# Optimization experiments

Hardware: AMD Instinct MI355X
Metric: run time of the kernel (lower is better)

## Reference

```python
import jax, jax.numpy as jnp
import numpy as np
from jax.scipy.linalg import expm

DIM = 2048        # state dimension (init arg `dim`)
M_STEPS = 8192    # kernel length (init arg `timestamp`)
DELTA = 0.01      # ZOH step size (init arg `delta`)
STAB = 1e-3       # stabilizer added to A before inversion (matches torch code)


def setup_inputs() -> dict:
    key = jax.random.key(0)
    k1, k2, k3 = jax.random.split(key, 3)
    # Match the torch init scaling so matrix_exp/inv stay well-conditioned.
    A = jnp.eye(DIM, dtype=jnp.float32) * -0.01 \
        + jax.random.normal(k1, (DIM, DIM), dtype=jnp.float32) * 0.001
    B = jax.random.normal(k2, (DIM, 1), dtype=jnp.float32) * 0.01
    C = jax.random.normal(k3, (1, DIM), dtype=jnp.float32) * 0.01
    return {"A": A, "B": B, "C": C, "M": M_STEPS}


def reference(A, B, C, M):
    dim = A.shape[0]
    I = jnp.eye(dim, dtype=A.dtype)
    # --- ZOH discretization (torch._zoh_discretize) ---
    A_bar = expm(DELTA * A)                         # [dim, dim]
    A_inv = jnp.linalg.inv(A + STAB * I)            # [dim, dim]
    B_bar = A_inv @ (A_bar - I) @ (DELTA * B)       # [dim, 1]

    # --- kernel power iteration (torch._compute_K_bar) ---
    # K[t] = C @ A_bar^t @ B_bar. Since B_bar is a vector, the serial
    # matrix-power loop reduces to M sequential matvecs (same math).
    def step(x, _):
        term = (C @ x)[0, 0]        # scalar K_t
        return A_bar @ x, term      # advance state: A_bar^{t+1} B_bar

    _, terms = jax.lax.scan(step, B_bar, None, length=M)  # [M]
    K_bar = terms[::-1][None, :]    # flip along time, shape [1, M]
    return K_bar
```

## Files before the change

### kernel.cpp

```cpp
#include <hip/hip_runtime.h>


#define DIMN 2048
#define MSTEPS 8192
#define RSPLIT 91
#define NSTEPS 90
#define NN ((size_t)DIMN * DIMN)
#define SCRD ((size_t)(1024*1024 + 512*512 + 256*256 + 128*128 + 64*64))
#define NBLK 32

__global__ __launch_bounds__(256)
void k_combine4(float* out,
                const float* i1, float c1, const float* i2, float c2,
                const float* i3, float c3, const float* i4, float c4,
                float dval)
{
  const int total = DIMN * DIMN;
  for (int idx = blockIdx.x * 256 + threadIdx.x; idx < total; idx += gridDim.x * 256) {
    float v = 0.f;
    if (i1) v = fmaf(c1, i1[idx], v);
    if (i2) v = fmaf(c2, i2[idx], v);
    if (i3) v = fmaf(c3, i3[idx], v);
    if (i4) v = fmaf(c4, i4[idx], v);
    if ((idx >> 11) == (idx & 2047)) v += dval;
    out[idx] = v;
  }
}

__global__ __launch_bounds__(256)
void k_fill64(const float* __restrict__ A, double* __restrict__ M)
{
  const int total = DIMN * DIMN;
  for (int idx = blockIdx.x * 256 + threadIdx.x; idx < total; idx += gridDim.x * 256) {
    double v = (double)A[idx];
    if ((idx >> 11) == (idx & 2047)) v += 1e-3;
    M[idx] = v;
  }
}

#define GBM 128
#define GBN 128
#define GBK 8
__global__ __launch_bounds__(256)
void k_gemm(const float* __restrict__ A, int lda,
            const float* __restrict__ B, int ldb,
            float* C, int ldc, int K, float alpha,
            const float* E1, int ld1, float c1,
            const float* E2, int ld2, float c2,
            const float* E3, int ld3, float c3,
            float dval)
{
  __shared__ float As[GBK][GBM];
  __shared__ float Bs[GBK][GBN];
  const int tid = threadIdx.x;
  const int tx = tid & 15, ty = tid >> 4;
  const int brow = blockIdx.y * GBM, bcol = blockIdx.x * GBN;

  const int arow = tid >> 1, ac0 = (tid & 1) * 4;
  const int brw  = tid >> 5, bc0 = (tid & 31) * 4;

  const float* Aptr = A + (size_t)(brow + arow) * lda + ac0;
  const float* Bptr = B + (size_t)brw * ldb + (bcol + bc0);

  float4 aPre = *(const float4*)Aptr;
  float4 bPre = *(const float4*)Bptr;

  float acc[8][8];
#pragma unroll
  for (int i = 0; i < 8; ++i)
#pragma unroll
    for (int j = 0; j < 8; ++j) acc[i][j] = 0.f;

  const int nk = K / GBK;
  for (int kt = 0; kt < nk; ++kt) {
    As[ac0 + 0][arow] = aPre.x;
    As[ac0 + 1][arow] = aPre.y;
    As[ac0 + 2][arow] = aPre.z;
    As[ac0 + 3][arow] = aPre.w;
    *(float4*)&Bs[brw][bc0] = bPre;
    __syncthreads();
    if (kt + 1 < nk) {
      aPre = *(const float4*)(Aptr + (size_t)(kt + 1) * GBK);
      bPre = *(const float4*)(Bptr + (size_t)(kt + 1) * GBK * ldb);
    }
#pragma unroll
    for (int kk = 0; kk < GBK; ++kk) {
      float a[8], b[8];
      *(float4*)&a[0] = *(const float4*)&As[kk][ty * 8];
      *(float4*)&a[4] = *(const float4*)&As[kk][ty * 8 + 4];
      *(float4*)&b[0] = *(const float4*)&Bs[kk][tx * 8];
      *(float4*)&b[4] = *(const float4*)&Bs[kk][tx * 8 + 4];
#pragma unroll
      for (int i = 0; i < 8; ++i)
#pragma unroll
        for (int j = 0; j < 8; ++j)
          acc[i][j] = fmaf(a[i], b[j], acc[i][j]);
    }
    __syncthreads();
  }
#pragma unroll
  for (int i = 0; i < 8; ++i) {
    const int gi = brow + ty * 8 + i;
#pragma unroll
    for (int j = 0; j < 8; ++j) {
      const int gj = bcol + tx * 8 + j;
      float v = alpha * acc[i][j];
      if (E1) v = fmaf(c1, E1[(size_t)gi * ld1 + gj], v);
      if (E2) v = fmaf(c2, E2[(size_t)gi * ld2 + gj], v);
      if (E3) v = fmaf(c3, E3[(size_t)gi * ld3 + gj], v);
      if (gi == gj) v += dval;
      C[(size_t)gi * ldc + gj] = v;
    }
  }
}

#define DBM 64
#define DBK 8
__global__ __launch_bounds__(256)
void k_dgemm(const double* __restrict__ A, int lda,
             const double* __restrict__ B, int ldb,
             double* C, int ldc, int K, double alpha,
             const double* E1, int ld1, double c1)
{
  __shared__ double As[DBK][DBM];
  __shared__ double Bs[DBK][DBM];
  const int tid = threadIdx.x;
  const int tx = tid & 15, ty = tid >> 4;
  const int brow = blockIdx.y * DBM, bcol = blockIdx.x * DBM;

  const int arow = tid >> 2, ac0 = (tid & 3) * 2;
  const int brw  = tid >> 5, bc0 = (tid & 31) * 2;

  const double* Aptr = A + (size_t)(brow + arow) * lda + ac0;
  const double* Bptr = B + (size_t)brw * ldb + (bcol + bc0);

  double2 aPre = *(const double2*)Aptr;
  double2 bPre = *(const double2*)Bptr;

  double acc[4][4];
#pragma unroll
  for (int i = 0; i < 4; ++i)
#pragma unroll
    for (int j = 0; j < 4; ++j) acc[i][j] = 0.0;

  const int nk = K / DBK;
  for (int kt = 0; kt < nk; ++kt) {
    As[ac0 + 0][arow] = aPre.x;
    As[ac0 + 1][arow] = aPre.y;
    Bs[brw][bc0 + 0] = bPre.x;
    Bs[brw][bc0 + 1] = bPre.y;
    __syncthreads();
    if (kt + 1 < nk) {
      aPre = *(const double2*)(Aptr + (size_t)(kt + 1) * DBK);
      bPre = *(const double2*)(Bptr + (size_t)(kt + 1) * DBK * ldb);
    }
#pragma unroll
    for (int kk = 0; kk < DBK; ++kk) {
      double a[4], b[4];
#pragma unroll
      for (int i = 0; i < 4; ++i) a[i] = As[kk][ty * 4 + i];
#pragma unroll
      for (int j = 0; j < 4; ++j) b[j] = Bs[kk][tx * 4 + j];
#pragma unroll
      for (int i = 0; i < 4; ++i)
#pragma unroll
        for (int j = 0; j < 4; ++j)
          acc[i][j] = fma(a[i], b[j], acc[i][j]);
    }
    __syncthreads();
  }
#pragma unroll
  for (int i = 0; i < 4; ++i) {
    const int gi = brow + ty * 4 + i;
#pragma unroll
    for (int j = 0; j < 4; ++j) {
      const int gj = bcol + tx * 4 + j;
      double v = alpha * acc[i][j];
      if (E1) v = fma(c1, E1[(size_t)gi * ld1 + gj], v);
      C[(size_t)gi * ldc + gj] = v;
    }
  }
}

__global__ __launch_bounds__(256)
void k_transpose(const float* __restrict__ in, float* __restrict__ out)
{
  __shared__ float t[32][33];
  const int bx = blockIdx.x * 32, by = blockIdx.y * 32;
  const int lx = threadIdx.x, ly = threadIdx.y;
  for (int dy = 0; dy < 32; dy += 8)
    t[ly + dy][lx] = in[(size_t)(by + ly + dy) * DIMN + bx + lx];
  __syncthreads();
  for (int dy = 0; dy < 32; dy += 8)
    out[(size_t)(bx + ly + dy) * DIMN + by + lx] = t[lx][ly + dy];
}

__global__ __launch_bounds__(1024)
void k_gj64(const double* __restrict__ M, int ldm, double* __restrict__ W, int ldw)
{
  __shared__ double a[64][130];
  __shared__ double s_rpv;
  __shared__ int s_rp;
  __shared__ int s_used[64];
  __shared__ int s_r[64];
  const int tid = threadIdx.x;
  for (int idx = tid; idx < 64 * 64; idx += 1024) {
    const int r = idx >> 6, c = idx & 63;
    a[r][c] = M[(size_t)r * ldm + c];
    a[r][64 + c] = (r == c) ? 1.0 : 0.0;
  }
  if (tid < 64) s_used[tid] = 0;
  __syncthreads();

  const int c = tid & 127;
  const int rg = tid >> 7;

  for (int p = 0; p < 64; ++p) {
    if (tid < 64) {
      double v = s_used[tid] ? -1.0 : fabs(a[tid][p]);
      int bi = tid;
      for (int off = 32; off; off >>= 1) {
        const double ov = __shfl_down(v, off);
        const int oi = __shfl_down(bi, off);
        if (ov > v) { v = ov; bi = oi; }
      }
      if (tid == 0) {
        s_rp = bi; s_r[p] = bi; s_used[bi] = 1;
        s_rpv = 1.0 / a[bi][p];
      }
    }
    __syncthreads();
    const int rp = s_rp;
    const double prs = a[rp][c] * s_rpv;
    double pv[8];
#pragma unroll
    for (int k = 0; k < 8; ++k) pv[k] = a[rg * 8 + k][p];
    __syncthreads();
#pragma unroll
    for (int k = 0; k < 8; ++k) {
      const int i = rg * 8 + k;
      a[i][c] = (i == rp) ? prs : fma(-pv[k], prs, a[i][c]);
    }
    __syncthreads();
  }

  for (int idx = tid; idx < 64 * 64; idx += 1024) {
    const int r = idx >> 6, cc = idx & 63;
    W[(size_t)r * ldw + cc] = a[s_r[r]][64 + cc];
  }
}

__global__ __launch_bounds__(256)
void k_setrow(double* __restrict__ Rpan, const double* __restrict__ Dinv,
              double* __restrict__ M, int p)
{
  const int idx = blockIdx.x * 256 + threadIdx.x;
  const int r = idx >> 11, c = idx & 2047;
  double v;
  if ((c >> 6) == p) {
    v = Dinv[r * 64 + (c & 63)];
    Rpan[(size_t)r * DIMN + c] = v;
  } else {
    v = Rpan[(size_t)r * DIMN + c];
  }
  M[(size_t)(p * 64 + r) * DIMN + c] = v;
}

__global__ __launch_bounds__(256)
void k_colprep(double* __restrict__ Cpan, double* __restrict__ M, int p)
{
  const int idx = blockIdx.x * 256 + threadIdx.x;
  const int i = idx >> 6, k = idx & 63;
  const bool inP = (i >> 6) == p;
  const size_t mo = (size_t)i * DIMN + p * 64 + k;
  double v = 0.0;
  if (!inP) { v = M[mo]; M[mo] = 0.0; }
  Cpan[idx] = v;
}

__global__ __launch_bounds__(256)
void k_mv(const float* __restrict__ Mat, const double* __restrict__ vin,
          double* vout, const double* vadd, double alpha)
{
  const int lane = threadIdx.x & 63;
  const int row = blockIdx.x * 4 + (threadIdx.x >> 6);
  const float* mrow = Mat + (size_t)row * DIMN;
  double acc = 0.0;
  for (int p = 0; p < DIMN; p += 256) {
    const float4 m = *(const float4*)&mrow[p + lane * 4];
    const double* vp = &vin[p + lane * 4];
    acc += (double)m.x * vp[0] + (double)m.y * vp[1] + (double)m.z * vp[2] + (double)m.w * vp[3];
  }
  for (int off = 32; off; off >>= 1) acc += __shfl_down(acc, off);
  if (lane == 0) vout[row] = alpha * acc + (vadd ? vadd[row] : 0.0);
}

__global__ __launch_bounds__(256)
void k_mv64(const double* __restrict__ W, const double* __restrict__ vin,
            double* vout, const double* vadd, double alpha)
{
  const int lane = threadIdx.x & 63;
  const int row = blockIdx.x * 4 + (threadIdx.x >> 6);
  const double* mrow = W + (size_t)row * DIMN;
  double acc = 0.0;
  for (int p = 0; p < DIMN; p += 256) {
    const int idx = p + lane * 4;
    const double2 m0 = *(const double2*)&mrow[idx];
    const double2 m1 = *(const double2*)&mrow[idx + 2];
    acc += m0.x * vin[idx] + m0.y * vin[idx + 1] + m1.x * vin[idx + 2] + m1.y * vin[idx + 3];
  }
  for (int off = 32; off; off >>= 1) acc += __shfl_down(acc, off);
  if (lane == 0) vout[row] = alpha * acc + (vadd ? vadd[row] : 0.0);
}

__global__ __launch_bounds__(256)
void k_mvres(const float* __restrict__ A, const double* __restrict__ x,
             const double* __restrict__ y, double* r)
{
  const int lane = threadIdx.x & 63;
  const int row = blockIdx.x * 4 + (threadIdx.x >> 6);
  const float* mrow = A + (size_t)row * DIMN;
  double acc = 0.0;
  for (int p = 0; p < DIMN; p += 256) {
    const float4 m = *(const float4*)&mrow[p + lane * 4];
    const double* vp = &x[p + lane * 4];
    acc += (double)m.x * vp[0] + (double)m.y * vp[1] + (double)m.z * vp[2] + (double)m.w * vp[3];
  }
  for (int off = 32; off; off >>= 1) acc += __shfl_down(acc, off);
  if (lane == 0) r[row] = y[row] - acc - 1e-3 * x[row];
}

__global__ __launch_bounds__(256)
void k_chain(const float* __restrict__ E, const float* __restrict__ vin, float* __restrict__ vout,
             const float* __restrict__ ERT, const float* __restrict__ uin, float* __restrict__ uout)
{
  const int lane = threadIdx.x & 63;
  const int w = threadIdx.x >> 6;
  const int b = blockIdx.x;
  const float* mrow; const float* xin; float* xout; int row;
  if (b < 512) { row = b * 4 + w; mrow = E + (size_t)row * DIMN; xin = vin; xout = vout; }
  else { row = (b - 512) * 4 + w; mrow = ERT + (size_t)row * DIMN; xin = uin; xout = uout; }
  float acc = 0.f;
  for (int p = 0; p < DIMN; p += 256) {
    const float4 m = *(const float4*)&mrow[p + lane * 4];
    const float* vp = &xin[p + lane * 4];
    acc = fmaf(m.x, vp[0], acc);
    acc = fmaf(m.y, vp[1], acc);
    acc = fmaf(m.z, vp[2], acc);
    acc = fmaf(m.w, vp[3], acc);
  }
  for (int off = 32; off; off >>= 1) acc += __shfl_down(acc, off);
  if (lane == 0) xout[row] = xin[row] + acc;
}

__global__ __launch_bounds__(256)
void k_terms(const float* __restrict__ U, const float* __restrict__ V, float* __restrict__ out)
{
  const int lane = threadIdx.x & 63;
  const int t = blockIdx.x * 4 + (threadIdx.x >> 6);
  const int j = t / RSPLIT, i = t - j * RSPLIT;
  const float* u = U + (size_t)j * DIMN;
  const float* v = V + (size_t)i * DIMN;
  float acc = 0.f;
  for (int p = 0; p < DIMN; p += 256) {
    const float4 a4 = *(const float4*)&u[p + lane * 4];
    const float4 b4 = *(const float4*)&v[p + lane * 4];
    acc = fmaf(a4.x, b4.x, acc); acc = fmaf(a4.y, b4.y, acc);
    acc = fmaf(a4.z, b4.z, acc); acc = fmaf(a4.w, b4.w, acc);
  }
  for (int off = 32; off; off >>= 1) acc += __shfl_down(acc, off);
  if (lane == 0) out[MSTEPS - 1 - t] = acc;
}

__global__ void k_vecinit(const float* __restrict__ B, double* __restrict__ b64,
                          const float* __restrict__ Cv, float* __restrict__ U0)
{
  const int i = blockIdx.x * 256 + threadIdx.x;
  if (i < DIMN) { b64[i] = 0.01 * (double)B[i]; U0[i] = Cv[i]; }
}
__global__ void k_v0(const double* __restrict__ x64, float* __restrict__ V0)
{
  const int i = blockIdx.x * 256 + threadIdx.x;
  if (i < DIMN) V0[i] = (float)x64[i];
}

static inline void gemm(hipStream_t s, const float* A, int lda, const float* B, int ldb,
                        float* C, int ldc, int m, int n, int k, float alpha,
                        const float* E1 = nullptr, int ld1 = 0, float c1 = 0.f,
                        const float* E2 = nullptr, int ld2 = 0, float c2 = 0.f,
                        const float* E3 = nullptr, int ld3 = 0, float c3 = 0.f,
                        float dval = 0.f)
{
  dim3 grid(n / GBN, m / GBM), block(256);
  k_gemm<<<grid, block, 0, s>>>(A, lda, B, ldb, C, ldc, k, alpha,
                                E1, ld1, c1, E2, ld2, c2, E3, ld3, c3, dval);
}

static void invert_gj64(hipStream_t s, double* M, double* Dinv, double* Cpan, double* Rpan)
{
  for (int p = 0; p < NBLK; ++p) {
    double* Mrow = M + (size_t)p * 64 * DIMN;
    k_gj64<<<dim3(1), dim3(1024), 0, s>>>(Mrow + p * 64, DIMN, Dinv, 64);
    k_dgemm<<<dim3(32, 1), dim3(256), 0, s>>>(Dinv, 64, Mrow, DIMN, Rpan, DIMN, 64, 1.0,
                                              nullptr, 0, 0.0);
    k_setrow<<<dim3(512), dim3(256), 0, s>>>(Rpan, Dinv, M, p);
    k_colprep<<<dim3(512), dim3(256), 0, s>>>(Cpan, M, p);
    k_dgemm<<<dim3(32, 32), dim3(256), 0, s>>>(Cpan, 64, Rpan, DIMN, M, DIMN, 64, -1.0,
                                               M, DIMN, 1.0);
  }
}

extern "C" void kernel_launch(void* const* d_in, const int* in_sizes, int n_in,
                              void* d_out, int out_size, void* d_ws, size_t ws_size,
                              hipStream_t stream)
{
  const float* dA = (const float*)d_in[0];
  const float* dB = (const float*)d_in[1];
  const float* dC = (const float*)d_in[2];
  float* out = (float*)d_out;

  float* fb = (float*)d_ws;
  float* Ebuf = fb;
  float* t1 = fb + NN;
  float* t2 = t1 + NN;
  float* t3 = t2 + NN;
  float* t4 = t3 + NN;
  double* M64 = (double*)t1;
  double* scr64 = (double*)(fb + 5 * NN);
  double* Dinv = scr64;
  double* Cpan = Dinv + 64 * 64;
  double* Rpan = Cpan + (size_t)DIMN * 64;
  double* y64 = Rpan + (size_t)DIMN * 64;
  double* x64 = y64 + DIMN;
  double* r64 = x64 + DIMN;
  double* b64 = r64 + DIMN;
  float* V  = (float*)(b64 + DIMN);
  float* Uc = V + (size_t)RSPLIT * DIMN;

  const size_t needed = 5 * NN * 4
                        + (64 * 64 + 2 * (size_t)DIMN * 64 + 4 * (size_t)DIMN) * 8
                        + (size_t)(2 * RSPLIT) * DIMN * 4;
  if (ws_size < needed) return;

  const float* NUL = nullptr;
  dim3 cb(256), cg(2048);

  k_fill64<<<cg, cb, 0, stream>>>(dA, M64);
  invert_gj64(stream, M64, Dinv, Cpan, Rpan);

  gemm(stream, dA, DIMN, dA, DIMN, t3, DIMN, DIMN, DIMN, DIMN, 0.8281f);
  k_combine4<<<cg, cb, 0, stream>>>(Ebuf, t3, (float)(5e-5 / 0.8281), dA, 0.01f,
                                    NUL, 0, NUL, 0, 0.f);

  k_vecinit<<<dim3(8), cb, 0, stream>>>(dB, b64, dC, Uc);
  k_mv<<<dim3(512), cb, 0, stream>>>(Ebuf, b64, y64, (const double*)nullptr, 1.0);
  k_mv64<<<dim3(512), cb, 0, stream>>>(M64, y64, x64, (const double*)nullptr, 1.0);
  for (int it = 0; it < 2; ++it) {
    k_mvres<<<dim3(512), cb, 0, stream>>>(dA, x64, y64, r64);
    k_mv64<<<dim3(512), cb, 0, stream>>>(M64, r64, x64, x64, 1.0);
  }
  k_v0<<<dim3(8), cb, 0, stream>>>(x64, V);

  k_combine4<<<cg, cb, 0, stream>>>(t4, dA, 0.91f / 6.f, t3, 1.f / 24.f,
                                    NUL, 0, NUL, 0, 0.f);
  gemm(stream, t3, DIMN, t4, DIMN, t1, DIMN, DIMN, DIMN, DIMN, 1.f,
       t3, DIMN, 0.5f, dA, DIMN, 0.91f);
  k_transpose<<<dim3(64, 64), dim3(32, 8), 0, stream>>>(t1, t2);

  for (int s = 0; s < NSTEPS; ++s) {
    k_chain<<<dim3(1024), cb, 0, stream>>>(Ebuf, V + (size_t)s * DIMN, V + (size_t)(s + 1) * DIMN,
                                           t2, Uc + (size_t)s * DIMN, Uc + (size_t)(s + 1) * DIMN);
  }
  k_terms<<<dim3(2048), cb, 0, stream>>>(Uc, V, out);
}
```

Before: 5.200 ms.

## Use split-bf16 MFMA GEMMs, fuse row scaling, streamline block Gauss-Jordan pivoting

Replaces the scalar fp32 SIMT GEMM with a three-product split-bf16 (hi/lo) MFMA GEMM that reads operands from pre-split and pre-transposed bf16 buffers. This moves the two large 2048^3 products onto matrix cores. It also fuses the Dinv·row-panel dgemm with the row write-back into a single kernel. In the 64x64 Gauss-Jordan kernel, the serial per-step pivot search is replaced by a partial max computed during the update, which removes a sync per pivot. One residual-refinement iteration of the solve is dropped, which trades some solve accuracy for fewer passes, and the split-bf16 GEMM carries a small precision risk relative to fp32.

```diff
diff --git a/kernel.cpp b/kernel.cpp
--- a/kernel.cpp
+++ b/kernel.cpp
@@ -1,4 +1,5 @@
 #include <hip/hip_runtime.h>
+#include <hip/hip_bf16.h>
 
 
 #define DIMN 2048
@@ -6,8 +7,20 @@
 #define RSPLIT 91
 #define NSTEPS 90
 #define NN ((size_t)DIMN * DIMN)
-#define SCRD ((size_t)(1024*1024 + 512*512 + 256*256 + 128*128 + 64*64))
 #define NBLK 32
+#define ALD 40
+
+typedef short short8 __attribute__((ext_vector_type(8)));
+typedef float f32x4 __attribute__((ext_vector_type(4)));
+
+__device__ inline void split1(float x, unsigned short& h, unsigned short& l)
+{
+  __hip_bfloat16 b = __float2bfloat16(x);
+  h = *reinterpret_cast<unsigned short*>(&b);
+  float r = x - __bfloat162float(b);
+  __hip_bfloat16 b2 = __float2bfloat16(r);
+  l = *reinterpret_cast<unsigned short*>(&b2);
+}
 
 __global__ __launch_bounds__(256)
 void k_combine4(float* out,
@@ -38,78 +51,114 @@
   }
 }
 
-#define GBM 128
-#define GBN 128
-#define GBK 8
-__global__ __launch_bounds__(256)
-void k_gemm(const float* __restrict__ A, int lda,
-            const float* __restrict__ B, int ldb,
-            float* C, int ldc, int K, float alpha,
-            const float* E1, int ld1, float c1,
-            const float* E2, int ld2, float c2,
-            const float* E3, int ld3, float c3,
-            float dval)
-{
-  __shared__ float As[GBK][GBM];
-  __shared__ float Bs[GBK][GBN];
+__global__ __launch_bounds__(256)
+void k_split(const float* __restrict__ in, unsigned short* __restrict__ hi,
+             unsigned short* __restrict__ lo)
+{
+  const int i4 = blockIdx.x * 256 + threadIdx.x;
+  const float4 v = ((const float4*)in)[i4];
+  ushort4 h, l;
+  split1(v.x, h.x, l.x); split1(v.y, h.y, l.y);
+  split1(v.z, h.z, l.z); split1(v.w, h.w, l.w);
+  ((ushort4*)hi)[i4] = h;
+  ((ushort4*)lo)[i4] = l;
+}
+
+__global__ __launch_bounds__(256)
+void k_splitT(const float* __restrict__ in, unsigned short* __restrict__ hi,
+              unsigned short* __restrict__ lo)
+{
+  __shared__ float t[32][33];
+  const int bx = blockIdx.x * 32, by = blockIdx.y * 32;
+  const int lx = threadIdx.x, ly = threadIdx.y;
+  for (int dy = 0; dy < 32; dy += 8)
+    t[ly + dy][lx] = in[(size_t)(by + ly + dy) * DIMN + bx + lx];
+  __syncthreads();
+  for (int dy = 0; dy < 32; dy += 8) {
+    const size_t o = (size_t)(bx + ly + dy) * DIMN + by + lx;
+    unsigned short h, l;
+    split1(t[lx][ly + dy], h, l);
+    hi[o] = h; lo[o] = l;
+  }
+}
+
+__global__ __launch_bounds__(256)
+void k_gemm3(const unsigned short* __restrict__ Ahg, const unsigned short* __restrict__ Alg,
+             const unsigned short* __restrict__ Bhg, const unsigned short* __restrict__ Blg,
+             float* __restrict__ C, float alpha,
+             const float* E1, float c1, const float* E2, float c2)
+{
+  __shared__ unsigned short sAh[128 * ALD];
+  __shared__ unsigned short sAl[128 * ALD];
+  __shared__ unsigned short sBh[128 * ALD];
+  __shared__ unsigned short sBl[128 * ALD];
   const int tid = threadIdx.x;
-  const int tx = tid & 15, ty = tid >> 4;
-  const int brow = blockIdx.y * GBM, bcol = blockIdx.x * GBN;
-
-  const int arow = tid >> 1, ac0 = (tid & 1) * 4;
-  const int brw  = tid >> 5, bc0 = (tid & 31) * 4;
-
-  const float* Aptr = A + (size_t)(brow + arow) * lda + ac0;
-  const float* Bptr = B + (size_t)brw * ldb + (bcol + bc0);
-
-  float4 aPre = *(const float4*)Aptr;
-  float4 bPre = *(const float4*)Bptr;
-
-  float acc[8][8];
-#pragma unroll
-  for (int i = 0; i < 8; ++i)
-#pragma unroll
-    for (int j = 0; j < 8; ++j) acc[i][j] = 0.f;
-
-  const int nk = K / GBK;
+  const int wid = tid >> 6, lane = tid & 63;
+  const int lr = lane & 15, lg = lane >> 4;
+  const int wm = wid >> 1, wn = wid & 1;
+  const int brow = blockIdx.y * 128, bcol = blockIdx.x * 128;
+  const int sr = tid >> 1, sh = (tid & 1) * 16;
+
+  const unsigned short* gAh = Ahg + (size_t)(brow + sr) * DIMN + sh;
+  const unsigned short* gAl = Alg + (size_t)(brow + sr) * DIMN + sh;
+  const unsigned short* gBh = Bhg + (size_t)(bcol + sr) * DIMN + sh;
+  const unsigned short* gBl = Blg + (size_t)(bcol + sr) * DIMN + sh;
+
+  f32x4 acc[4][4];
+#pragma unroll
+  for (int mf = 0; mf < 4; ++mf)
+#pragma unroll
+    for (int nf = 0; nf < 4; ++nf) acc[mf][nf] = (f32x4){0.f, 0.f, 0.f, 0.f};
+
+  uint4 pa0 = *(const uint4*)gAh;      uint4 pa1 = *(const uint4*)(gAh + 8);
+  uint4 pb0 = *(const uint4*)gAl;      uint4 pb1 = *(const uint4*)(gAl + 8);
+  uint4 pc0 = *(const uint4*)gBh;      uint4 pc1 = *(const uint4*)(gBh + 8);
+  uint4 pd0 = *(const uint4*)gBl;      uint4 pd1 = *(const uint4*)(gBl + 8);
+
+  const int nk = DIMN / 32;
   for (int kt = 0; kt < nk; ++kt) {
-    As[ac0 + 0][arow] = aPre.x;
-    As[ac0 + 1][arow] = aPre.y;
-    As[ac0 + 2][arow] = aPre.z;
-    As[ac0 + 3][arow] = aPre.w;
-    *(float4*)&Bs[brw][bc0] = bPre;
+    *(uint4*)&sAh[sr * ALD + sh] = pa0;  *(uint4*)&sAh[sr * ALD + sh + 8] = pa1;
+    *(uint4*)&sAl[sr * ALD + sh] = pb0;  *(uint4*)&sAl[sr * ALD + sh + 8] = pb1;
+    *(uint4*)&sBh[sr * ALD + sh] = pc0;  *(uint4*)&sBh[sr * ALD + sh + 8] = pc1;
+    *(uint4*)&sBl[sr * ALD + sh] = pd0;  *(uint4*)&sBl[sr * ALD + sh + 8] = pd1;
     __syncthreads();
     if (kt + 1 < nk) {
-      aPre = *(const float4*)(Aptr + (size_t)(kt + 1) * GBK);
-      bPre = *(const float4*)(Bptr + (size_t)(kt + 1) * GBK * ldb);
-    }
-#pragma unroll
-    for (int kk = 0; kk < GBK; ++kk) {
-      float a[8], b[8];
-      *(float4*)&a[0] = *(const float4*)&As[kk][ty * 8];
-      *(float4*)&a[4] = *(const float4*)&As[kk][ty * 8 + 4];
-      *(float4*)&b[0] = *(const float4*)&Bs[kk][tx * 8];
-      *(float4*)&b[4] = *(const float4*)&Bs[kk][tx * 8 + 4];
-#pragma unroll
-      for (int i = 0; i < 8; ++i)
-#pragma unroll
-        for (int j = 0; j < 8; ++j)
-          acc[i][j] = fmaf(a[i], b[j], acc[i][j]);
-    }
-    __syncthreads();
-  }
-#pragma unroll
-  for (int i = 0; i < 8; ++i) {
-    const int gi = brow + ty * 8 + i;
-#pragma unroll
-    for (int j = 0; j < 8; ++j) {
-      const int gj = bcol + tx * 8 + j;
-      float v = alpha * acc[i][j];
-      if (E1) v = fmaf(c1, E1[(size_t)gi * ld1 + gj], v);
-      if (E2) v = fmaf(c2, E2[(size_t)gi * ld2 + gj], v);
-      if (E3) v = fmaf(c3, E3[(size_t)gi * ld3 + gj], v);
-      if (gi == gj) v += dval;
-      C[(size_t)gi * ldc + gj] = v;
+      const int o = (kt + 1) * 32;
+      pa0 = *(const uint4*)(gAh + o);  pa1 = *(const uint4*)(gAh + o + 8);
+      pb0 = *(const uint4*)(gAl + o);  pb1 = *(const uint4*)(gAl + o + 8);
+      pc0 = *(const uint4*)(gBh + o);  pc1 = *(const uint4*)(gBh + o + 8);
+      pd0 = *(const uint4*)(gBl + o);  pd1 = *(const uint4*)(gBl + o + 8);
+    }
+#pragma unroll
+    for (int mf = 0; mf < 4; ++mf) {
+      const int ar = 64 * wm + 16 * mf + lr;
+      const short8 ah = *(const short8*)&sAh[ar * ALD + lg * 8];
+      const short8 al = *(const short8*)&sAl[ar * ALD + lg * 8];
+#pragma unroll
+      for (int nf = 0; nf < 4; ++nf) {
+        const int br = 64 * wn + 16 * nf + lr;
+        const short8 bh = *(const short8*)&sBh[br * ALD + lg * 8];
+        const short8 bl = *(const short8*)&sBl[br * ALD + lg * 8];
+        acc[mf][nf] = __builtin_amdgcn_mfma_f32_16x16x32_bf16(ah, bh, acc[mf][nf], 0, 0, 0);
+        acc[mf][nf] = __builtin_amdgcn_mfma_f32_16x16x32_bf16(ah, bl, acc[mf][nf], 0, 0, 0);
+        acc[mf][nf] = __builtin_amdgcn_mfma_f32_16x16x32_bf16(al, bh, acc[mf][nf], 0, 0, 0);
+      }
+    }
+    __syncthreads();
+  }
+#pragma unroll
+  for (int mf = 0; mf < 4; ++mf) {
+#pragma unroll
+    for (int nf = 0; nf < 4; ++nf) {
+      const int col = bcol + 64 * wn + 16 * nf + lr;
+#pragma unroll
+      for (int i = 0; i < 4; ++i) {
+        const int row = brow + 64 * wm + 16 * mf + 4 * lg + i;
+        float v = alpha * acc[mf][nf][i];
+        if (E1) v = fmaf(c1, E1[(size_t)row * DIMN + col], v);
+        if (E2) v = fmaf(c2, E2[(size_t)row * DIMN + col], v);
+        C[(size_t)row * DIMN + col] = v;
+      }
     }
   }
 }
@@ -183,55 +232,109 @@
 }
 
 __global__ __launch_bounds__(256)
-void k_transpose(const float* __restrict__ in, float* __restrict__ out)
-{
-  __shared__ float t[32][33];
-  const int bx = blockIdx.x * 32, by = blockIdx.y * 32;
-  const int lx = threadIdx.x, ly = threadIdx.y;
-  for (int dy = 0; dy < 32; dy += 8)
-    t[ly + dy][lx] = in[(size_t)(by + ly + dy) * DIMN + bx + lx];
-  __syncthreads();
-  for (int dy = 0; dy < 32; dy += 8)
-    out[(size_t)(bx + ly + dy) * DIMN + by + lx] = t[lx][ly + dy];
+void k_rowscale(const double* __restrict__ Dinv, const double* __restrict__ Mrow,
+                double* __restrict__ Rpan, double* __restrict__ M, int p)
+{
+  __shared__ double As[DBK][DBM];
+  __shared__ double Bs[DBK][DBM];
+  const int tid = threadIdx.x;
+  const int tx = tid & 15, ty = tid >> 4;
+  const int bcol = blockIdx.x * DBM;
+
+  const int arow = tid >> 2, ac0 = (tid & 3) * 2;
+  const int brw  = tid >> 5, bc0 = (tid & 31) * 2;
+
+  const double* Aptr = Dinv + (size_t)arow * 64 + ac0;
+  const double* Bptr = Mrow + (size_t)brw * DIMN + (bcol + bc0);
+
+  double2 aPre = *(const double2*)Aptr;
+  double2 bPre = *(const double2*)Bptr;
+
+  double acc[4][4];
+#pragma unroll
+  for (int i = 0; i < 4; ++i)
+#pragma unroll
+    for (int j = 0; j < 4; ++j) acc[i][j] = 0.0;
+
+  for (int kt = 0; kt < 8; ++kt) {
+    As[ac0 + 0][arow] = aPre.x;
+    As[ac0 + 1][arow] = aPre.y;
+    Bs[brw][bc0 + 0] = bPre.x;
+    Bs[brw][bc0 + 1] = bPre.y;
+    __syncthreads();
+    if (kt + 1 < 8) {
+      aPre = *(const double2*)(Aptr + (size_t)(kt + 1) * DBK);
+      bPre = *(const double2*)(Bptr + (size_t)(kt + 1) * DBK * DIMN);
+    }
+#pragma unroll
+    for (int kk = 0; kk < DBK; ++kk) {
+      double a[4], b[4];
+#pragma unroll
+      for (int i = 0; i < 4; ++i) a[i] = As[kk][ty * 4 + i];
+#pragma unroll
+      for (int j = 0; j < 4; ++j) b[j] = Bs[kk][tx * 4 + j];
+#pragma unroll
+      for (int i = 0; i < 4; ++i)
+#pragma unroll
+        for (int j = 0; j < 4; ++j)
+          acc[i][j] = fma(a[i], b[j], acc[i][j]);
+    }
+    __syncthreads();
+  }
+  const bool pivcol = (bcol >> 6) == p;
+#pragma unroll
+  for (int i = 0; i < 4; ++i) {
+    const int gi = ty * 4 + i;
+#pragma unroll
+    for (int j = 0; j < 4; ++j) {
+      const int gj = bcol + tx * 4 + j;
+      double v = pivcol ? Dinv[(size_t)gi * 64 + (gj & 63)] : acc[i][j];
+      Rpan[(size_t)gi * DIMN + gj] = v;
+      M[(size_t)(p * 64 + gi) * DIMN + gj] = v;
+    }
+  }
 }
 
 __global__ __launch_bounds__(1024)
 void k_gj64(const double* __restrict__ M, int ldm, double* __restrict__ W, int ldw)
 {
   __shared__ double a[64][130];
-  __shared__ double s_rpv;
-  __shared__ int s_rp;
-  __shared__ int s_used[64];
+  __shared__ double part_v[8];
+  __shared__ int part_i[8];
   __shared__ int s_r[64];
   const int tid = threadIdx.x;
-  for (int idx = tid; idx < 64 * 64; idx += 1024) {
-    const int r = idx >> 6, c = idx & 63;
-    a[r][c] = M[(size_t)r * ldm + c];
-    a[r][64 + c] = (r == c) ? 1.0 : 0.0;
-  }
-  if (tid < 64) s_used[tid] = 0;
-  __syncthreads();
-
   const int c = tid & 127;
   const int rg = tid >> 7;
 
+  for (int idx = tid; idx < 64 * 64; idx += 1024) {
+    const int r = idx >> 6, cc = idx & 63;
+    a[r][cc] = M[(size_t)r * ldm + cc];
+    a[r][64 + cc] = (r == cc) ? 1.0 : 0.0;
+  }
+  unsigned long long used = 0ULL;
+  __syncthreads();
+  if (c == 0) {
+    double bv = -1.0; int bi = rg * 8;
+#pragma unroll
+    for (int k = 0; k < 8; ++k) {
+      const double v = fabs(a[rg * 8 + k][0]);
+      if (v > bv) { bv = v; bi = rg * 8 + k; }
+    }
+    part_v[rg] = bv; part_i[rg] = bi;
+  }
+  __syncthreads();
+
   for (int p = 0; p < 64; ++p) {
-    if (tid < 64) {
-      double v = s_used[tid] ? -1.0 : fabs(a[tid][p]);
-      int bi = tid;
-      for (int off = 32; off; off >>= 1) {
-        const double ov = __shfl_down(v, off);
-        const int oi = __shfl_down(bi, off);
-        if (ov > v) { v = ov; bi = oi; }
-      }
-      if (tid == 0) {
-        s_rp = bi; s_r[p] = bi; s_used[bi] = 1;
-        s_rpv = 1.0 / a[bi][p];
-      }
-    }
-    __syncthreads();
-    const int rp = s_rp;
-    const double prs = a[rp][c] * s_rpv;
+    double bv = part_v[0]; int rp = part_i[0];
+#pragma unroll
+    for (int g = 1; g < 8; ++g) {
+      const double v = part_v[g];
+      if (v > bv) { bv = v; rp = part_i[g]; }
+    }
+    used |= (1ULL << rp);
+    if (tid == 0) s_r[p] = rp;
+    const double rpv = 1.0 / a[rp][p];
+    const double prs = a[rp][c] * rpv;
     double pv[8];
 #pragma unroll
     for (int k = 0; k < 8; ++k) pv[k] = a[rg * 8 + k][p];
@@ -241,6 +344,16 @@
       const int i = rg * 8 + k;
       a[i][c] = (i == rp) ? prs : fma(-pv[k], prs, a[i][c]);
     }
+    if (p < 63 && c == p + 1) {
+      double mbv = -1.0; int mbi = rg * 8;
+#pragma unroll
+      for (int k = 0; k < 8; ++k) {
+        const int i = rg * 8 + k;
+        const double v = ((used >> i) & 1ULL) ? -1.0 : fabs(a[i][c]);
+        if (v > mbv) { mbv = v; mbi = i; }
+      }
+      part_v[rg] = mbv; part_i[rg] = mbi;
+    }
     __syncthreads();
   }
 
@@ -248,22 +361,6 @@
     const int r = idx >> 6, cc = idx & 63;
     W[(size_t)r * ldw + cc] = a[s_r[r]][64 + cc];
   }
-}
-
-__global__ __launch_bounds__(256)
-void k_setrow(double* __restrict__ Rpan, const double* __restrict__ Dinv,
-              double* __restrict__ M, int p)
-{
-  const int idx = blockIdx.x * 256 + threadIdx.x;
-  const int r = idx >> 11, c = idx & 2047;
-  double v;
-  if ((c >> 6) == p) {
-    v = Dinv[r * 64 + (c & 63)];
-    Rpan[(size_t)r * DIMN + c] = v;
-  } else {
-    v = Rpan[(size_t)r * DIMN + c];
-  }
-  M[(size_t)(p * 64 + r) * DIMN + c] = v;
 }
 
 __global__ __launch_bounds__(256)
@@ -328,6 +425,19 @@
   }
   for (int off = 32; off; off >>= 1) acc += __shfl_down(acc, off);
   if (lane == 0) r[row] = y[row] - acc - 1e-3 * x[row];
+}
+
+__global__ __launch_bounds__(256)
+void k_transpose(const float* __restrict__ in, float* __restrict__ out)
+{
+  __shared__ float t[32][33];
+  const int bx = blockIdx.x * 32, by = blockIdx.y * 32;
+  const int lx = threadIdx.x, ly = threadIdx.y;
+  for (int dy = 0; dy < 32; dy += 8)
+    t[ly + dy][lx] = in[(size_t)(by + ly + dy) * DIMN + bx + lx];
+  __syncthreads();
+  for (int dy = 0; dy < 32; dy += 8)
+    out[(size_t)(bx + ly + dy) * DIMN + by + lx] = t[lx][ly + dy];
 }
 
 __global__ __launch_bounds__(256)
@@ -382,32 +492,6 @@
 {
   const int i = blockIdx.x * 256 + threadIdx.x;
   if (i < DIMN) V0[i] = (float)x64[i];
-}
-
-static inline void gemm(hipStream_t s, const float* A, int lda, const float* B, int ldb,
-                        float* C, int ldc, int m, int n, int k, float alpha,
-                        const float* E1 = nullptr, int ld1 = 0, float c1 = 0.f,
-                        const float* E2 = nullptr, int ld2 = 0, float c2 = 0.f,
-                        const float* E3 = nullptr, int ld3 = 0, float c3 = 0.f,
-                        float dval = 0.f)
-{
-  dim3 grid(n / GBN, m / GBM), block(256);
-  k_gemm<<<grid, block, 0, s>>>(A, lda, B, ldb, C, ldc, k, alpha,
-                                E1, ld1, c1, E2, ld2, c2, E3, ld3, c3, dval);
-}
-
-static void invert_gj64(hipStream_t s, double* M, double* Dinv, double* Cpan, double* Rpan)
-{
-  for (int p = 0; p < NBLK; ++p) {
-    double* Mrow = M + (size_t)p * 64 * DIMN;
-    k_gj64<<<dim3(1), dim3(1024), 0, s>>>(Mrow + p * 64, DIMN, Dinv, 64);
-    k_dgemm<<<dim3(32, 1), dim3(256), 0, s>>>(Dinv, 64, Mrow, DIMN, Rpan, DIMN, 64, 1.0,
-                                              nullptr, 0, 0.0);
-    k_setrow<<<dim3(512), dim3(256), 0, s>>>(Rpan, Dinv, M, p);
-    k_colprep<<<dim3(512), dim3(256), 0, s>>>(Cpan, M, p);
-    k_dgemm<<<dim3(32, 32), dim3(256), 0, s>>>(Cpan, 64, Rpan, DIMN, M, DIMN, 64, -1.0,
-                                               M, DIMN, 1.0);
-  }
 }
 
 extern "C" void kernel_launch(void* const* d_in, const int* in_sizes, int n_in,
@@ -445,31 +529,46 @@
   const float* NUL = nullptr;
   dim3 cb(256), cg(2048);
 
-  k_fill64<<<cg, cb, 0, stream>>>(dA, M64);
-  invert_gj64(stream, M64, Dinv, Cpan, Rpan);
-
-  gemm(stream, dA, DIMN, dA, DIMN, t3, DIMN, DIMN, DIMN, DIMN, 0.8281f);
+  unsigned short* Ah  = (unsigned short*)t4;   unsigned short* Al  = Ah + NN;
+  unsigned short* Ath = (unsigned short*)Ebuf; unsigned short* Atl = Ath + NN;
+  unsigned short* Y2h = (unsigned short*)t1;   unsigned short* Y2l = Y2h + NN;
+  unsigned short* Hth = (unsigned short*)t2;   unsigned short* Htl = Hth + NN;
+
+  k_split<<<dim3(4096), cb, 0, stream>>>(dA, Ah, Al);
+  k_splitT<<<dim3(64, 64), dim3(32, 8), 0, stream>>>(dA, Ath, Atl);
+  k_gemm3<<<dim3(16, 16), cb, 0, stream>>>(Ah, Al, Ath, Atl, t3, 0.8281f,
+                                           NUL, 0.f, NUL, 0.f);
   k_combine4<<<cg, cb, 0, stream>>>(Ebuf, t3, (float)(5e-5 / 0.8281), dA, 0.01f,
                                     NUL, 0, NUL, 0, 0.f);
+
+  k_fill64<<<cg, cb, 0, stream>>>(dA, M64);
+  for (int p = 0; p < NBLK; ++p) {
+    double* Mrow = M64 + (size_t)p * 64 * DIMN;
+    k_gj64<<<dim3(1), dim3(1024), 0, stream>>>(Mrow + p * 64, DIMN, Dinv, 64);
+    k_rowscale<<<dim3(32), cb, 0, stream>>>(Dinv, Mrow, Rpan, M64, p);
+    k_colprep<<<dim3(512), cb, 0, stream>>>(Cpan, M64, p);
+    k_dgemm<<<dim3(32, 32), cb, 0, stream>>>(Cpan, 64, Rpan, DIMN, M64, DIMN, 64, -1.0,
+                                             M64, DIMN, 1.0);
+  }
 
   k_vecinit<<<dim3(8), cb, 0, stream>>>(dB, b64, dC, Uc);
   k_mv<<<dim3(512), cb, 0, stream>>>(Ebuf, b64, y64, (const double*)nullptr, 1.0);
   k_mv64<<<dim3(512), cb, 0, stream>>>(M64, y64, x64, (const double*)nullptr, 1.0);
-  for (int it = 0; it < 2; ++it) {
-    k_mvres<<<dim3(512), cb, 0, stream>>>(dA, x64, y64, r64);
-    k_mv64<<<dim3(512), cb, 0, stream>>>(M64, r64, x64, x64, 1.0);
-  }
+  k_mvres<<<dim3(512), cb, 0, stream>>>(dA, x64, y64, r64);
+  k_mv64<<<dim3(512), cb, 0, stream>>>(M64, r64, x64, x64, 1.0);
   k_v0<<<dim3(8), cb, 0, stream>>>(x64, V);
 
   k_combine4<<<cg, cb, 0, stream>>>(t4, dA, 0.91f / 6.f, t3, 1.f / 24.f,
                                     NUL, 0, NUL, 0, 0.f);
-  gemm(stream, t3, DIMN, t4, DIMN, t1, DIMN, DIMN, DIMN, DIMN, 1.f,
-       t3, DIMN, 0.5f, dA, DIMN, 0.91f);
-  k_transpose<<<dim3(64, 64), dim3(32, 8), 0, stream>>>(t1, t2);
+  k_split<<<dim3(4096), cb, 0, stream>>>(t3, Y2h, Y2l);
+  k_splitT<<<dim3(64, 64), dim3(32, 8), 0, stream>>>(t4, Hth, Htl);
+  k_gemm3<<<dim3(16, 16), cb, 0, stream>>>(Y2h, Y2l, Hth, Htl, t3, 1.f,
+                                           t3, 0.5f, dA, 0.91f);
+  k_transpose<<<dim3(64, 64), dim3(32, 8), 0, stream>>>(t3, t4);
 
   for (int s = 0; s < NSTEPS; ++s) {
     k_chain<<<dim3(1024), cb, 0, stream>>>(Ebuf, V + (size_t)s * DIMN, V + (size_t)(s + 1) * DIMN,
-                                           t2, Uc + (size_t)s * DIMN, Uc + (size_t)(s + 1) * DIMN);
+                                           t4, Uc + (size_t)s * DIMN, Uc + (size_t)(s + 1) * DIMN);
   }
   k_terms<<<dim3(2048), cb, 0, stream>>>(Uc, V, out);
 }
```

Result: slower. 6.031 ms (+16.0%).
